# Optimization experiments

Measured on AMD Instinct MI355X. Metric: run time of the kernel, lower is better.

The kernel has to match this reference:

```python
import jax, jax.numpy as jnp
import numpy as np

EPS = 1e-7
B, C, IMG = 1024, 3, 32
NCLASS = 10
N_IN, L_IN, L_OUT = 64, 16, 16   # primary caps: 64 capsules of length 16; digit caps length 16
R_ITER = 3


def squash(c, axis):
    dot = jnp.sum(c * c, axis=axis, keepdims=True)
    return dot / (1.0 + dot) / jnp.sqrt(dot + EPS) * c


def conv2d(x, w, b, stride):
    y = jax.lax.conv_general_dilated(x, w, (stride, stride), 'VALID',
                                     dimension_numbers=('NCHW', 'OIHW', 'NCHW'))
    return y + b[None, :, None, None]


def setup_inputs() -> dict:
    key = jax.random.key(0)
    ks = jax.random.split(key, 16)
    inp = {
        'x': jax.random.uniform(ks[0], (B, C, IMG, IMG), dtype=jnp.float32),
        'y': jax.random.randint(ks[1], (B,), 0, NCLASS, dtype=jnp.int64),
        'conv1_w': 0.05 * jax.random.normal(ks[2], (128, C, 3, 3), jnp.float32),
        'conv1_b': jnp.zeros((128,), jnp.float32),
        'conv2_w': 0.05 * jax.random.normal(ks[3], (256, 128, 5, 5), jnp.float32),
        'conv2_b': jnp.zeros((256,), jnp.float32),
        'conv3_w': 0.05 * jax.random.normal(ks[4], (256, 256, 5, 5), jnp.float32),
        'conv3_b': jnp.zeros((256,), jnp.float32),
        'caps_w': 0.05 * jax.random.normal(ks[5], (N_IN, NCLASS, L_IN, L_OUT), jnp.float32),
        'caps_b': 0.05 * jax.random.normal(ks[6], (NCLASS, L_OUT), jnp.float32),
        'fc1_w': 0.05 * jax.random.normal(ks[7], (512, NCLASS * L_OUT), jnp.float32),
        'fc1_b': jnp.zeros((512,), jnp.float32),
        'fc2_w': 0.05 * jax.random.normal(ks[8], (1024, 512), jnp.float32),
        'fc2_b': jnp.zeros((1024,), jnp.float32),
        'fc3_w': 0.05 * jax.random.normal(ks[9], (IMG * IMG * C, 1024), jnp.float32),
        'fc3_b': jnp.zeros((IMG * IMG * C,), jnp.float32),
    }
    return inp


def reference(x, y, conv1_w, conv1_b, conv2_w, conv2_b, conv3_w, conv3_b,
              caps_w, caps_b, fc1_w, fc1_b, fc2_w, fc2_b, fc3_w, fc3_b):
    # CNN blocks
    h = jax.nn.relu(conv2d(x, conv1_w, conv1_b, 2))   # [B,128,15,15]
    h = jax.nn.relu(conv2d(h, conv2_w, conv2_b, 2))   # [B,256,6,6]
    h = jax.nn.relu(conv2d(h, conv3_w, conv3_b, 1))   # [B,256,2,2]

    # Primary capsules: [B,64,16], squashed along capsule-length axis
    prim = squash(h.reshape(h.shape[0], N_IN, L_IN), axis=-1)

    # u_hat[b,i,o,j] = sum_k W[i,o,k,j] * prim[b,i,k]  -> [B,64,10,16]
    u_hat = jnp.einsum('bik,iokj->bioj', prim, caps_w)
    u_hat_det = jax.lax.stop_gradient(u_hat)

    b_ij = jnp.zeros((h.shape[0], N_IN, NCLASS), dtype=u_hat.dtype)
    v = None
    for r in range(R_ITER):
        c_ij = jax.nn.softmax(b_ij, axis=2)           # over output capsules
        uh = u_hat if r == R_ITER - 1 else u_hat_det
        s = jnp.einsum('bio,bioj->boj', c_ij, uh) + caps_b   # [B,10,16]
        v = squash(s, axis=-1)
        if r < R_ITER - 1:
            agree = jnp.einsum('bioj,boj->bio', u_hat_det, jax.lax.stop_gradient(v))
            b_ij = b_ij + agree

    # capsule lengths: [B,10,1,1]
    v_lengths = jnp.sqrt(jnp.sum(v * v, axis=-1, keepdims=True) + EPS)[..., None]

    # reconstruction (mask by true label one-hot)
    one_hot = jax.nn.one_hot(y, NCLASS, dtype=v.dtype)       # [B,10]
    masked = (v * one_hot[:, :, None]).reshape(v.shape[0], NCLASS * L_OUT)
    h1 = jax.nn.relu(masked @ fc1_w.T + fc1_b)
    h2 = jax.nn.relu(h1 @ fc2_w.T + fc2_b)
    decoded = jax.nn.sigmoid(h2 @ fc3_w.T + fc3_b)           # [B,3072]
    return (v_lengths, decoded)
```

## Files before the change

### kernel.cpp

```cpp
#include <hip/hip_runtime.h>
#include <hip/hip_bf16.h>
#include <math.h>

#define EPSF 1e-7f

typedef __attribute__((ext_vector_type(8))) short bhalf8;
typedef __attribute__((ext_vector_type(4))) float floatx4;

__global__ __launch_bounds__(256) void conv1_kernel(
    const float* __restrict__ x, const float* __restrict__ w,
    const float* __restrict__ bias, __hip_bfloat16* __restrict__ out)
{
  __shared__ float wl[3456];
  __shared__ float bl[128];
  const int b = blockIdx.x;
  const int t = threadIdx.x;
  for (int i = t; i < 3456; i += 256) wl[i] = w[i];
  if (t < 128) bl[t] = bias[t];
  __syncthreads();
  if (t >= 225) return;
  const int py = t / 15, px = t % 15;
  const float* xb = x + b * 3072;
  float win[27];
#pragma unroll
  for (int c = 0; c < 3; ++c)
#pragma unroll
    for (int ky = 0; ky < 3; ++ky)
#pragma unroll
      for (int kx = 0; kx < 3; ++kx)
        win[c*9 + ky*3 + kx] = xb[c*1024 + (py*2 + ky)*32 + (px*2 + kx)];
#pragma unroll 1
  for (int oc0 = 0; oc0 < 128; oc0 += 32) {
    __hip_bfloat16 hv[32];
#pragma unroll
    for (int oc = 0; oc < 32; ++oc) {
      const float* wp = &wl[(oc0 + oc)*27];
      float acc = bl[oc0 + oc];
#pragma unroll
      for (int q = 0; q < 27; ++q) acc = fmaf(win[q], wp[q], acc);
      hv[oc] = __float2bfloat16(fmaxf(acc, 0.f));
    }
    uint4* dst = (uint4*)&out[((size_t)b*225 + t)*128 + oc0];
    const uint4* src = (const uint4*)hv;
#pragma unroll
    for (int q = 0; q < 4; ++q) dst[q] = src[q];
  }
}

__global__ __launch_bounds__(256) void wtrans_kernel(
    const float* __restrict__ w, __hip_bfloat16* __restrict__ wt)
{
  int i = blockIdx.x*256 + threadIdx.x;
  int s = i >> 13, r = i & 8191;
  int oc = r >> 5, kq = r & 31;
  int k = s*32 + kq;
  int tap = k >> 7, ic = k & 127;
  wt[i] = __float2bfloat16(w[(oc*128 + ic)*25 + tap]);
}

__global__ __launch_bounds__(256) void wtrans3_kernel(
    const float* __restrict__ w, __hip_bfloat16* __restrict__ wt)
{
  int i = blockIdx.x*256 + threadIdx.x;
  int s = i >> 14, r = i & 16383;
  int oc = r >> 6, kq = r & 63;
  int k = s*64 + kq;
  int tap = k >> 8, ic = k & 255;
  wt[i] = __float2bfloat16(w[(oc*256 + ic)*25 + tap]);
}

__global__ __launch_bounds__(256) void wtrans_caps_kernel(
    const float* __restrict__ cw, __hip_bfloat16* __restrict__ cwt)
{
  int i2 = blockIdx.x*256 + threadIdx.x;
  int k  = i2 & 15, j = (i2 >> 4) & 15, io = i2 >> 8;
  cwt[i2] = __float2bfloat16(cw[(io*16 + k)*16 + j]);
}

__global__ __launch_bounds__(256) void wtrans_fc1_kernel(
    const float* __restrict__ w, float* __restrict__ wt)
{
  int i = blockIdx.x*256 + threadIdx.x;
  int j = i >> 9, n = i & 511;
  wt[i] = w[n*160 + j];
}

__global__ __launch_bounds__(256) void cast_bf16_kernel(
    const float* __restrict__ src, __hip_bfloat16* __restrict__ dst, int n)
{
  int i = blockIdx.x*256 + threadIdx.x;
  if (i < n) dst[i] = __float2bfloat16(src[i]);
}

__global__ __launch_bounds__(1024) void conv2_mfma_kernel(
    const __hip_bfloat16* __restrict__ a,
    const __hip_bfloat16* __restrict__ wt,
    const float* __restrict__ bias,
    __hip_bfloat16* __restrict__ out)
{
  __shared__ __align__(16) unsigned short Il[2*225*136];
  const int b0   = blockIdx.x * 2;
  const int t    = threadIdx.x;
  const int lane = t & 63;
  const int w    = t >> 6;
  const int n    = lane & 15;
  const int g    = lane >> 4;

  const char* gB = (const char*)wt + (w*16 + n)*64 + g*16;
  bhalf8 bb[4];
#pragma unroll
  for (int ss = 0; ss < 4; ++ss)
    bb[ss] = *(const bhalf8*)(gB + ss*16384);

  for (int i = t; i < 7200; i += 1024) {
    int img = (i >= 3600);
    int r = i - img*3600;
    int p = r >> 4, c = r & 15;
    uint4 v = *(const uint4*)((const char*)a +
              (((size_t)(b0+img)*225 + p)*256 + c*16));
    int csw = (c + (p >> 1) + (p >> 5)) & 15;
    *(uint4*)((char*)Il + ((img*225 + p)*136 + csw*8)*2) = v;
  }

  int rowb[5], pixb[5];
#pragma unroll
  for (int mt = 0; mt < 5; ++mt) {
    int m  = mt*16 + n;
    int mm = (m < 72) ? m : 0;
    int img = (mm >= 36);
    int pos = mm - img*36;
    int py = pos/6, px = pos - py*6;
    pixb[mt] = 30*py + 2*px;
    rowb[mt] = img*225*136;
  }

  floatx4 acc[5];
#pragma unroll
  for (int mt = 0; mt < 5; ++mt) acc[mt] = (floatx4){0.f, 0.f, 0.f, 0.f};

  __syncthreads();

  int s = 0;
#pragma unroll 1
  for (int ky = 0; ky < 5; ++ky) {
#pragma unroll 1
    for (int kx = 0; kx < 5; ++kx) {
      const int dpix = ky*15 + kx;
      int prow[5], pqv[5];
#pragma unroll
      for (int mt = 0; mt < 5; ++mt) {
        int p = pixb[mt] + dpix;
        prow[mt] = rowb[mt] + p*136;
        pqv[mt]  = (p >> 1) + (p >> 5);
      }
#pragma unroll
      for (int icq = 0; icq < 4; ++icq) {
        const int scur = s + icq;
#pragma unroll
        for (int mt = 0; mt < 5; ++mt) {
          int csw = ((icq*4 + g) + pqv[mt]) & 15;
          bhalf8 af = *(const bhalf8*)((const char*)Il +
                       (prow[mt] + csw*8)*2);
          acc[mt] = __builtin_amdgcn_mfma_f32_16x16x32_bf16(
              af, bb[icq], acc[mt], 0, 0, 0);
        }
        {
          const int spre = (scur + 4 <= 99) ? (scur + 4) : 99;
          bb[icq] = *(const bhalf8*)(gB + spre*16384);
        }
      }
      s += 4;
    }
  }

  const float bv = bias[w*16 + n];
#pragma unroll
  for (int mt = 0; mt < 5; ++mt) {
#pragma unroll
    for (int r = 0; r < 4; ++r) {
      int m = mt*16 + g*4 + r;
      if (m < 72) {
        int img = (m >= 36);
        int pos = m - img*36;
        out[(((size_t)(b0+img)*36 + pos)*256 + w*16 + n)] =
            __float2bfloat16(fmaxf(acc[mt][r] + bv, 0.f));
      }
    }
  }
}

__global__ __launch_bounds__(512) void conv3_mfma_kernel(
    const __hip_bfloat16* __restrict__ a,
    const __hip_bfloat16* __restrict__ wt,
    float* __restrict__ pout)
{
  __shared__ __align__(16) unsigned short Il[16*1448];
  const int b0   = blockIdx.x * 16;
  const int kq   = blockIdx.y;
  const int t    = threadIdx.x;
  const int lane = t & 63;
  const int w    = t >> 6;
  const int n    = lane & 15;
  const int g    = lane >> 4;

  for (int i = t; i < 2304; i += 512) {
    int img = i / 144, r = i - img*144;
    int p = r >> 2, c = r & 3;
    uint4 v = *(const uint4*)((const char*)a +
              ((((size_t)(b0+img)*36 + p) << 9) + kq*64 + c*16));
    *(uint4*)((char*)Il + (img*1448 + p*40 + c*8)*2) = v;
  }

  const char* gB = (const char*)wt + (size_t)(w*32 + n)*128 +
                   (kq & 1)*64 + g*16;
  const int kqs = kq >> 1;
  bhalf8 b00, b01, b10, b11;
  b00 = *(const bhalf8*)(gB + (size_t)(0*4 + kqs)*32768);
  b01 = *(const bhalf8*)(gB + (size_t)(0*4 + kqs)*32768 + 2048);
  b10 = *(const bhalf8*)(gB + (size_t)(1*4 + kqs)*32768);
  b11 = *(const bhalf8*)(gB + (size_t)(1*4 + kqs)*32768 + 2048);

  const int d = n >> 2, pos = n & 3;
  const int pb = (pos >> 1)*6 + (pos & 1);
  int ab[4];
#pragma unroll
  for (int mt = 0; mt < 4; ++mt)
    ab[mt] = ((mt*4 + d)*1448 + pb*40 + g*8) * 2;

  floatx4 acc[4][2];
#pragma unroll
  for (int mt = 0; mt < 4; ++mt)
#pragma unroll
    for (int nt = 0; nt < 2; ++nt)
      acc[mt][nt] = (floatx4){0.f, 0.f, 0.f, 0.f};

  __syncthreads();

  int toff = 0, kx = 0;
#pragma unroll 1
  for (int tap = 0; tap < 24; tap += 2) {
#pragma unroll
    for (int mt = 0; mt < 4; ++mt) {
      bhalf8 av = *(const bhalf8*)((const char*)Il + ab[mt] + toff*80);
      acc[mt][0] = __builtin_amdgcn_mfma_f32_16x16x32_bf16(av, b00, acc[mt][0], 0, 0, 0);
      acc[mt][1] = __builtin_amdgcn_mfma_f32_16x16x32_bf16(av, b01, acc[mt][1], 0, 0, 0);
    }
    b00 = *(const bhalf8*)(gB + (size_t)((tap+2)*4 + kqs)*32768);
    b01 = *(const bhalf8*)(gB + (size_t)((tap+2)*4 + kqs)*32768 + 2048);
    if (++kx == 5) { kx = 0; toff += 2; } else ++toff;
#pragma unroll
    for (int mt = 0; mt < 4; ++mt) {
      bhalf8 av = *(const bhalf8*)((const char*)Il + ab[mt] + toff*80);
      acc[mt][0] = __builtin_amdgcn_mfma_f32_16x16x32_bf16(av, b10, acc[mt][0], 0, 0, 0);
      acc[mt][1] = __builtin_amdgcn_mfma_f32_16x16x32_bf16(av, b11, acc[mt][1], 0, 0, 0);
    }
    {
      const int tpre = (tap + 3 <= 24) ? (tap + 3) : 24;
      b10 = *(const bhalf8*)(gB + (size_t)(tpre*4 + kqs)*32768);
      b11 = *(const bhalf8*)(gB + (size_t)(tpre*4 + kqs)*32768 + 2048);
    }
    if (++kx == 5) { kx = 0; toff += 2; } else ++toff;
  }
#pragma unroll
  for (int mt = 0; mt < 4; ++mt) {
    bhalf8 av = *(const bhalf8*)((const char*)Il + ab[mt] + toff*80);
    acc[mt][0] = __builtin_amdgcn_mfma_f32_16x16x32_bf16(av, b00, acc[mt][0], 0, 0, 0);
    acc[mt][1] = __builtin_amdgcn_mfma_f32_16x16x32_bf16(av, b01, acc[mt][1], 0, 0, 0);
  }

  float* po = pout + (size_t)kq*1048576;
#pragma unroll
  for (int mt = 0; mt < 4; ++mt) {
#pragma unroll
    for (int r = 0; r < 4; ++r) {
      int m = mt*16 + g*4 + r;
      int img = m >> 2, p2 = m & 3;
#pragma unroll
      for (int nt = 0; nt < 2; ++nt)
        po[((size_t)(b0+img)*256 + w*32 + nt*16 + n)*4 + p2] = acc[mt][nt][r];
    }
  }
}

__global__ __launch_bounds__(256) void caps_kernel(
    const float* __restrict__ pout, const __hip_bfloat16* __restrict__ cwt,
    const float* __restrict__ cb, const float* __restrict__ c3b,
    const int* __restrict__ y,
    const float* __restrict__ fc1wt, const float* __restrict__ fc1b,
    float* __restrict__ vlen, __hip_bfloat16* __restrict__ h1f)
{
  __shared__ float prim[1024];
  __shared__ float uh[10240];
  __shared__ float bij[640];
  __shared__ float cij[640];
  __shared__ float vv[160];
  const int b = blockIdx.x, t = threadIdx.x;
  {
    const float* pp = pout + (size_t)b*1024 + t*4;
    float4 s4 = *(const float4*)pp;
#pragma unroll
    for (int q = 1; q < 8; ++q) {
      float4 v = *(const float4*)(pp + (size_t)q*1048576);
      s4.x += v.x; s4.y += v.y; s4.z += v.z; s4.w += v.w;
    }
    const float bv = c3b[t];
    float4 h = make_float4(fmaxf(s4.x + bv, 0.f), fmaxf(s4.y + bv, 0.f),
                           fmaxf(s4.z + bv, 0.f), fmaxf(s4.w + bv, 0.f));
    float dd = h.x*h.x + h.y*h.y + h.z*h.z + h.w*h.w;
    dd += __shfl_xor(dd, 1);
    dd += __shfl_xor(dd, 2);
    float sc = dd / (1.f + dd) / sqrtf(dd + EPSF);
    float4 o4 = make_float4(h.x*sc, h.y*sc, h.z*sc, h.w*sc);
    *(float4*)&prim[t*4] = o4;
  }
  for (int f = t; f < 640; f += 256) bij[f] = 0.f;
  __syncthreads();
  for (int f = t; f < 10240; f += 256) {
    const int i = f / 160;
    const uint4* wv = (const uint4*)(cwt + (size_t)f*16);
    uint4 wa = wv[0], wb = wv[1];
    unsigned uw[8] = {wa.x, wa.y, wa.z, wa.w, wb.x, wb.y, wb.z, wb.w};
    const float* pp = prim + i*16;
    float s = 0.f;
#pragma unroll
    for (int q = 0; q < 8; ++q) {
      float lo = __uint_as_float(uw[q] << 16);
      float hi = __uint_as_float(uw[q] & 0xffff0000u);
      s = fmaf(pp[2*q],   lo, s);
      s = fmaf(pp[2*q+1], hi, s);
    }
    uh[f] = s;
  }
  __syncthreads();
  for (int r = 0; r < 3; ++r) {
    if (t < 64) {
      float e[10];
      float mx = -1e30f;
#pragma unroll
      for (int o = 0; o < 10; ++o) { e[o] = bij[t*10 + o]; mx = fmaxf(mx, e[o]); }
      float sum = 0.f;
#pragma unroll
      for (int o = 0; o < 10; ++o) { e[o] = expf(e[o] - mx); sum += e[o]; }
      float inv = 1.f / sum;
#pragma unroll
      for (int o = 0; o < 10; ++o) cij[t*10 + o] = e[o] * inv;
    }
    __syncthreads();
    if (t < 160) {
      const int o = t >> 4;
      float s = cb[t];
      for (int i = 0; i < 64; ++i) s = fmaf(cij[i*10 + o], uh[i*160 + t], s);
      float dd = s*s;
      dd += __shfl_xor(dd, 1); dd += __shfl_xor(dd, 2);
      dd += __shfl_xor(dd, 4); dd += __shfl_xor(dd, 8);
      float sc = dd / (1.f + dd) / sqrtf(dd + EPSF);
      vv[t] = s * sc;
      if (r == 2 && (t & 15) == 0)
        vlen[b*10 + o] = sqrtf(sc*sc*dd + EPSF);
    }
    __syncthreads();
    if (r < 2) {
      for (int f = t; f < 640; f += 256) {
        int i = f / 10, o = f % 10;
        const float* up = &uh[i*160 + o*16];
        const float* vp = &vv[o*16];
        float a = 0.f;
#pragma unroll
        for (int j = 0; j < 16; ++j) a = fmaf(up[j], vp[j], a);
        bij[f] += a;
      }
      __syncthreads();
    }
  }
  const int yb = y[b];
  const float* vy = &vv[yb*16];
  for (int nn = t; nn < 512; nn += 256) {
    float s = fc1b[nn];
#pragma unroll
    for (int k = 0; k < 16; ++k)
      s = fmaf(vy[k], fc1wt[(yb*16 + k)*512 + nn], s);
    h1f[b*512 + nn] = __float2bfloat16(fmaxf(s, 0.f));
  }
}

template<int ACT, int MT, int NT>
__global__ __launch_bounds__(256) void fc_mfma_kernel(
    const __hip_bfloat16* __restrict__ A,
    const __hip_bfloat16* __restrict__ W,
    const float* __restrict__ bias,
    void* __restrict__ outv, int M, int N, int K)
{
  const int t    = threadIdx.x;
  const int lane = t & 63;
  const int w    = t >> 6;
  const int wr   = w >> 1, wc = w & 1;
  const int n    = lane & 15, g = lane >> 4;
  const int m0   = blockIdx.x * (2*MT*16) + wr*(MT*16);
  const int n0   = blockIdx.y * (2*NT*16) + wc*(NT*16);
  const __hip_bfloat16* Ap = A + (size_t)(m0 + n)*K + g*8;
  const __hip_bfloat16* Wp = W + (size_t)(n0 + n)*K + g*8;
  const int steps = K >> 5;

  bhalf8 aa0[MT], aa1[MT], bb0[NT], bb1[NT];
#pragma unroll
  for (int mt = 0; mt < MT; ++mt) {
    aa0[mt] = *(const bhalf8*)(Ap + (size_t)mt*16*K);
    aa1[mt] = *(const bhalf8*)(Ap + (size_t)mt*16*K + 32);
  }
#pragma unroll
  for (int nt = 0; nt < NT; ++nt) {
    bb0[nt] = *(const bhalf8*)(Wp + (size_t)nt*16*K);
    bb1[nt] = *(const bhalf8*)(Wp + (size_t)nt*16*K + 32);
  }

  floatx4 acc[MT][NT];
#pragma unroll
  for (int mt = 0; mt < MT; ++mt)
#pragma unroll
    for (int nt = 0; nt < NT; ++nt)
      acc[mt][nt] = (floatx4){0.f, 0.f, 0.f, 0.f};

#pragma unroll 1
  for (int s = 0; s < steps; s += 2) {
#pragma unroll
    for (int mt = 0; mt < MT; ++mt)
#pragma unroll
      for (int nt = 0; nt < NT; ++nt)
        acc[mt][nt] = __builtin_amdgcn_mfma_f32_16x16x32_bf16(
            aa0[mt], bb0[nt], acc[mt][nt], 0, 0, 0);
    {
      const int spre = (s + 2 < steps) ? (s + 2) : s;
#pragma unroll
      for (int mt = 0; mt < MT; ++mt)
        aa0[mt] = *(const bhalf8*)(Ap + (size_t)mt*16*K + spre*32);
#pragma unroll
      for (int nt = 0; nt < NT; ++nt)
        bb0[nt] = *(const bhalf8*)(Wp + (size_t)nt*16*K + spre*32);
    }
#pragma unroll
    for (int mt = 0; mt < MT; ++mt)
#pragma unroll
      for (int nt = 0; nt < NT; ++nt)
        acc[mt][nt] = __builtin_amdgcn_mfma_f32_16x16x32_bf16(
            aa1[mt], bb1[nt], acc[mt][nt], 0, 0, 0);
    {
      const int spre = (s + 3 < steps) ? (s + 3) : (s + 1);
#pragma unroll
      for (int mt = 0; mt < MT; ++mt)
        aa1[mt] = *(const bhalf8*)(Ap + (size_t)mt*16*K + spre*32);
#pragma unroll
      for (int nt = 0; nt < NT; ++nt)
        bb1[nt] = *(const bhalf8*)(Wp + (size_t)nt*16*K + spre*32);
    }
  }

#pragma unroll
  for (int mt = 0; mt < MT; ++mt) {
#pragma unroll
    for (int r = 0; r < 4; ++r) {
      const int m = m0 + mt*16 + g*4 + r;
#pragma unroll
      for (int nt = 0; nt < NT; ++nt) {
        const int col = n0 + nt*16 + n;
        float v = acc[mt][nt][r] + bias[col];
        if (ACT == 0) {
          ((__hip_bfloat16*)outv)[(size_t)m*N + col] =
              __float2bfloat16(fmaxf(v, 0.f));
        } else {
          ((float*)outv)[(size_t)m*N + col] = 1.f / (1.f + expf(-v));
        }
      }
    }
  }
}

extern "C" void kernel_launch(void* const* d_in, const int* in_sizes, int n_in,
                              void* d_out, int out_size, void* d_ws, size_t ws_size,
                              hipStream_t stream) {
  const float* x       = (const float*)d_in[0];
  const int*   y       = (const int*)  d_in[1];
  const float* conv1_w = (const float*)d_in[2];
  const float* conv1_b = (const float*)d_in[3];
  const float* conv2_w = (const float*)d_in[4];
  const float* conv2_b = (const float*)d_in[5];
  const float* conv3_w = (const float*)d_in[6];
  const float* conv3_b = (const float*)d_in[7];
  const float* caps_w  = (const float*)d_in[8];
  const float* caps_b  = (const float*)d_in[9];
  const float* fc1_w   = (const float*)d_in[10];
  const float* fc1_b   = (const float*)d_in[11];
  const float* fc2_w   = (const float*)d_in[12];
  const float* fc2_b   = (const float*)d_in[13];
  const float* fc3_w   = (const float*)d_in[14];
  const float* fc3_b   = (const float*)d_in[15];
  float* out = (float*)d_out;
  float* ws  = (float*)d_ws;

  __hip_bfloat16* h1t   = (__hip_bfloat16*)ws;
  __hip_bfloat16* wt2   = (__hip_bfloat16*)(ws + 14745600);
  __hip_bfloat16* wt3   = (__hip_bfloat16*)(ws + 15155200);
  __hip_bfloat16* h2t   = (__hip_bfloat16*)(ws + 15974400);
  float*          pout  = ws + 20692992;
  __hip_bfloat16* h1f   = (__hip_bfloat16*)(ws + 29081600);
  __hip_bfloat16* h2f   = (__hip_bfloat16*)(ws + 29343744);
  __hip_bfloat16* wf2   = (__hip_bfloat16*)(ws + 29868032);
  __hip_bfloat16* wf3   = (__hip_bfloat16*)(ws + 30130176);
  __hip_bfloat16* cwt   = (__hip_bfloat16*)(ws + 31703040);
  float*          fc1wt = ws + 31784960;

  wtrans_kernel     <<<dim3(3200),  256, 0, stream>>>(conv2_w, wt2);
  wtrans3_kernel    <<<dim3(6400),  256, 0, stream>>>(conv3_w, wt3);
  wtrans_caps_kernel<<<dim3(640),   256, 0, stream>>>(caps_w, cwt);
  wtrans_fc1_kernel <<<dim3(320),   256, 0, stream>>>(fc1_w, fc1wt);
  cast_bf16_kernel  <<<dim3(2048),  256, 0, stream>>>(fc2_w, wf2, 524288);
  cast_bf16_kernel  <<<dim3(12288), 256, 0, stream>>>(fc3_w, wf3, 3145728);
  conv1_kernel<<<dim3(1024),       256, 0, stream>>>(x, conv1_w, conv1_b, h1t);
  conv2_mfma_kernel<<<dim3(512),  1024, 0, stream>>>(h1t, wt2, conv2_b, h2t);
  conv3_mfma_kernel<<<dim3(64, 8), 512, 0, stream>>>(h2t, wt3, pout);
  caps_kernel<<<dim3(1024),        256, 0, stream>>>(pout, cwt, caps_b, conv3_b,
                                                     y, fc1wt, fc1_b, out, h1f);
  fc_mfma_kernel<0,2,2><<<dim3(16, 16), 256, 0, stream>>>(
      h1f, wf2, fc2_b, h2f, 1024, 1024, 512);
  fc_mfma_kernel<1,2,2><<<dim3(16, 48), 256, 0, stream>>>(
      h2f, wf3, fc3_b, out + 10240, 1024, 3072, 1024);
}
```

Before: 373.7 us.

## Retile conv2 MFMA kernel to 4 images per block with channel-half staging

The conv2 implicit-GEMM kernel now processes 4 images per block instead of 2. Its 16 waves are split 2x8 over M and N, so each wave computes a 5x2 tile of 16x16 outputs and reuses each A fragment across two B fragments. The input channels are staged into LDS in two halves of 64 channels, with a matching reordered weight layout, which keeps the LDS footprint small despite the larger batch tile. This cuts per-output A reads and weight reloads, but adds an extra sync phase, an unbalanced fifth M-tile handled by one wave row, and half as many blocks.

Result: faster. 350.1 us (-6.3%).

```diff
diff --git a/kernel.cpp b/kernel.cpp
--- a/kernel.cpp
+++ b/kernel.cpp
@@ -53,8 +53,10 @@
   int i = blockIdx.x*256 + threadIdx.x;
   int s = i >> 13, r = i & 8191;
   int oc = r >> 5, kq = r & 31;
-  int k = s*32 + kq;
-  int tap = k >> 7, ic = k & 127;
+  int h = (s >= 50) ? 1 : 0;
+  int r2 = s - h*50;
+  int tap = r2 >> 1, q = r2 & 1;
+  int ic = h*64 + q*32 + kq;
   wt[i] = __float2bfloat16(w[(oc*128 + ic)*25 + tap]);
 }
 
@@ -98,92 +100,117 @@
     const float* __restrict__ bias,
     __hip_bfloat16* __restrict__ out)
 {
-  __shared__ __align__(16) unsigned short Il[2*225*136];
-  const int b0   = blockIdx.x * 2;
+  __shared__ __align__(16) unsigned short Il[4*225*64];
+  const int b0   = blockIdx.x * 4;
   const int t    = threadIdx.x;
   const int lane = t & 63;
   const int w    = t >> 6;
+  const int wm   = w >> 3;
+  const int wn   = w & 7;
   const int n    = lane & 15;
   const int g    = lane >> 4;
 
-  const char* gB = (const char*)wt + (w*16 + n)*64 + g*16;
-  bhalf8 bb[4];
-#pragma unroll
-  for (int ss = 0; ss < 4; ++ss)
-    bb[ss] = *(const bhalf8*)(gB + ss*16384);
-
-  for (int i = t; i < 7200; i += 1024) {
-    int img = (i >= 3600);
-    int r = i - img*3600;
-    int p = r >> 4, c = r & 15;
-    uint4 v = *(const uint4*)((const char*)a +
-              (((size_t)(b0+img)*225 + p)*256 + c*16));
-    int csw = (c + (p >> 1) + (p >> 5)) & 15;
-    *(uint4*)((char*)Il + ((img*225 + p)*136 + csw*8)*2) = v;
-  }
-
-  int rowb[5], pixb[5];
+  const char* gB = (const char*)wt + (wn*32 + n)*64 + g*16;
+  bhalf8 b00 = *(const bhalf8*)(gB);
+  bhalf8 b01 = *(const bhalf8*)(gB + 1024);
+  bhalf8 b10 = *(const bhalf8*)(gB + 16384);
+  bhalf8 b11 = *(const bhalf8*)(gB + 16384 + 1024);
+
+  int Abase[5], em[5];
 #pragma unroll
   for (int mt = 0; mt < 5; ++mt) {
-    int m  = mt*16 + n;
-    int mm = (m < 72) ? m : 0;
-    int img = (mm >= 36);
-    int pos = mm - img*36;
-    int py = pos/6, px = pos - py*6;
-    pixb[mt] = 30*py + 2*px;
-    rowb[mt] = img*225*136;
-  }
-
-  floatx4 acc[5];
-#pragma unroll
-  for (int mt = 0; mt < 5; ++mt) acc[mt] = (floatx4){0.f, 0.f, 0.f, 0.f};
-
-  __syncthreads();
+    int tile = wm*5 + mt;
+    int m = tile*16 + n;
+    if (m >= 144) m = 0;
+    int img = m / 36, pos = m - img*36;
+    int py = pos / 6, px = pos - py*6;
+    int pixb = 30*py + 2*px;
+    Abase[mt] = (img*225 + pixb) * 128;
+    em[mt] = g + (pixb >> 1);
+  }
+
+  floatx4 acc[5][2];
+#pragma unroll
+  for (int mt = 0; mt < 5; ++mt)
+#pragma unroll
+    for (int nt = 0; nt < 2; ++nt)
+      acc[mt][nt] = (floatx4){0.f, 0.f, 0.f, 0.f};
 
   int s = 0;
 #pragma unroll 1
-  for (int ky = 0; ky < 5; ++ky) {
+  for (int h = 0; h < 2; ++h) {
+    if (h) __syncthreads();
+    for (int i = t; i < 7200; i += 1024) {
+      int img = i / 1800;
+      int r = i - img*1800;
+      int p = r >> 3, c = r & 7;
+      uint4 v = *(const uint4*)((const char*)a +
+                ((size_t)(b0+img)*225 + p)*256 + h*128 + c*16);
+      int csw = (c + (p >> 1)) & 7;
+      *(uint4*)((char*)Il + (img*225 + p)*128 + csw*16) = v;
+    }
+    __syncthreads();
+
+    int dpix = 0, kx = 0;
 #pragma unroll 1
-    for (int kx = 0; kx < 5; ++kx) {
-      const int dpix = ky*15 + kx;
-      int prow[5], pqv[5];
-#pragma unroll
-      for (int mt = 0; mt < 5; ++mt) {
-        int p = pixb[mt] + dpix;
-        prow[mt] = rowb[mt] + p*136;
-        pqv[mt]  = (p >> 1) + (p >> 5);
-      }
-#pragma unroll
-      for (int icq = 0; icq < 4; ++icq) {
-        const int scur = s + icq;
-#pragma unroll
-        for (int mt = 0; mt < 5; ++mt) {
-          int csw = ((icq*4 + g) + pqv[mt]) & 15;
-          bhalf8 af = *(const bhalf8*)((const char*)Il +
-                       (prow[mt] + csw*8)*2);
-          acc[mt] = __builtin_amdgcn_mfma_f32_16x16x32_bf16(
-              af, bb[icq], acc[mt], 0, 0, 0);
-        }
-        {
-          const int spre = (scur + 4 <= 99) ? (scur + 4) : 99;
-          bb[icq] = *(const bhalf8*)(gB + spre*16384);
-        }
-      }
-      s += 4;
-    }
-  }
-
-  const float bv = bias[w*16 + n];
+    for (int tap = 0; tap < 25; ++tap) {
+      const int doff = dpix << 7;
+      const int duh  = dpix >> 1;
+      int a0[5];
+#pragma unroll
+      for (int mt = 0; mt < 5; ++mt)
+        a0[mt] = Abase[mt] + doff + (((em[mt] + duh) & 7) << 4);
+
+#pragma unroll
+      for (int mt = 0; mt < 4; ++mt) {
+        bhalf8 av = *(const bhalf8*)((const char*)Il + a0[mt]);
+        acc[mt][0] = __builtin_amdgcn_mfma_f32_16x16x32_bf16(av, b00, acc[mt][0], 0, 0, 0);
+        acc[mt][1] = __builtin_amdgcn_mfma_f32_16x16x32_bf16(av, b01, acc[mt][1], 0, 0, 0);
+      }
+      if (wm == 0) {
+        bhalf8 av = *(const bhalf8*)((const char*)Il + a0[4]);
+        acc[4][0] = __builtin_amdgcn_mfma_f32_16x16x32_bf16(av, b00, acc[4][0], 0, 0, 0);
+        acc[4][1] = __builtin_amdgcn_mfma_f32_16x16x32_bf16(av, b01, acc[4][1], 0, 0, 0);
+      }
+      {
+        const int spre = (s + 2 < 100) ? (s + 2) : 99;
+        b00 = *(const bhalf8*)(gB + (size_t)spre*16384);
+        b01 = *(const bhalf8*)(gB + (size_t)spre*16384 + 1024);
+      }
+#pragma unroll
+      for (int mt = 0; mt < 4; ++mt) {
+        bhalf8 av = *(const bhalf8*)((const char*)Il + (a0[mt] ^ 64));
+        acc[mt][0] = __builtin_amdgcn_mfma_f32_16x16x32_bf16(av, b10, acc[mt][0], 0, 0, 0);
+        acc[mt][1] = __builtin_amdgcn_mfma_f32_16x16x32_bf16(av, b11, acc[mt][1], 0, 0, 0);
+      }
+      if (wm == 0) {
+        bhalf8 av = *(const bhalf8*)((const char*)Il + (a0[4] ^ 64));
+        acc[4][0] = __builtin_amdgcn_mfma_f32_16x16x32_bf16(av, b10, acc[4][0], 0, 0, 0);
+        acc[4][1] = __builtin_amdgcn_mfma_f32_16x16x32_bf16(av, b11, acc[4][1], 0, 0, 0);
+      }
+      {
+        const int spre = (s + 3 < 100) ? (s + 3) : 99;
+        b10 = *(const bhalf8*)(gB + (size_t)spre*16384);
+        b11 = *(const bhalf8*)(gB + (size_t)spre*16384 + 1024);
+      }
+      s += 2;
+      if (kx == 4) { kx = 0; dpix += 11; } else { ++kx; ++dpix; }
+    }
+  }
+
+  const float bv0 = bias[wn*32 + n];
+  const float bv1 = bias[wn*32 + 16 + n];
 #pragma unroll
   for (int mt = 0; mt < 5; ++mt) {
-#pragma unroll
-    for (int r = 0; r < 4; ++r) {
-      int m = mt*16 + g*4 + r;
-      if (m < 72) {
-        int img = (m >= 36);
-        int pos = m - img*36;
-        out[(((size_t)(b0+img)*36 + pos)*256 + w*16 + n)] =
-            __float2bfloat16(fmaxf(acc[mt][r] + bv, 0.f));
+    if (mt < 4 || wm == 0) {
+      int tile = wm*5 + mt;
+#pragma unroll
+      for (int r = 0; r < 4; ++r) {
+        int m = tile*16 + g*4 + r;
+        int img = m / 36, pos = m - img*36;
+        size_t o = (((size_t)(b0+img)*36 + pos) << 8) + wn*32 + n;
+        out[o]      = __float2bfloat16(fmaxf(acc[mt][0][r] + bv0, 0.f));
+        out[o + 16] = __float2bfloat16(fmaxf(acc[mt][1][r] + bv1, 0.f));
       }
     }
   }
@@ -515,7 +542,7 @@
   cast_bf16_kernel  <<<dim3(2048),  256, 0, stream>>>(fc2_w, wf2, 524288);
   cast_bf16_kernel  <<<dim3(12288), 256, 0, stream>>>(fc3_w, wf3, 3145728);
   conv1_kernel<<<dim3(1024),       256, 0, stream>>>(x, conv1_w, conv1_b, h1t);
-  conv2_mfma_kernel<<<dim3(512),  1024, 0, stream>>>(h1t, wt2, conv2_b, h2t);
+  conv2_mfma_kernel<<<dim3(256),  1024, 0, stream>>>(h1t, wt2, conv2_b, h2t);
   conv3_mfma_kernel<<<dim3(64, 8), 512, 0, stream>>>(h2t, wt3, pout);
   caps_kernel<<<dim3(1024),        256, 0, stream>>>(pout, cwt, caps_b, conv3_b,
                                                      y, fc1wt, fc1_b, out, h1f);
```
